# Kernel tuning notes

Hardware: AMD Instinct MI355X
Metric: run time of the kernel (lower is better)

Reference implementation:

```python
import jax, jax.numpy as jnp
import numpy as np

N, E, G = 100000, 1600000, 16
GW = 128
EPS = 1e-5        # BatchNorm eps
MIN_SCORE = 0.1   # TopK min_score
TOL = 1e-7        # PyG topk tolerance
NEG = -1e9


def _seg_sum(v, idx, n):
    return jax.ops.segment_sum(v, idx, num_segments=n)


def _seg_max(v, idx, n):
    return jax.ops.segment_max(v, idx, num_segments=n)


def setup_inputs():
    ks = jax.random.split(jax.random.key(0), 32)
    inp = {}
    inp['x'] = jax.random.normal(ks[0], (N, 2), jnp.float32)
    inp['edge_index'] = jax.random.randint(ks[1], (2, E), 0, N, jnp.int32)
    inp['batch_index'] = jnp.sort(jax.random.randint(ks[2], (N,), 0, G, jnp.int32))
    inp['gcn_w'] = jax.random.normal(ks[3], (2, 1), jnp.float32) / np.sqrt(2.0)
    inp['gcn_b'] = jax.random.normal(ks[4], (1,), jnp.float32) * 0.1
    inp['topk_w'] = jax.random.normal(ks[5], (1,), jnp.float32)
    dims = [(2, GW), (GW, GW), (GW, GW)]
    j = 6
    for i, (din, dout) in enumerate(dims):
        s = 1.0 / np.sqrt(din)
        inp[f'cheb{i}_w0'] = jax.random.normal(ks[j], (din, dout), jnp.float32) * s; j += 1
        inp[f'cheb{i}_w1'] = jax.random.normal(ks[j], (din, dout), jnp.float32) * s; j += 1
        inp[f'cheb{i}_b'] = jax.random.normal(ks[j], (dout,), jnp.float32) * 0.1; j += 1
    inp['bn_gamma'] = jax.random.uniform(ks[j], (3, GW), jnp.float32) + 0.5; j += 1
    inp['bn_beta'] = jax.random.normal(ks[j], (3, GW), jnp.float32) * 0.1; j += 1
    inp['bn_mean'] = jax.random.normal(ks[j], (3, GW), jnp.float32) * 0.1; j += 1
    inp['bn_var'] = jax.random.uniform(ks[j], (3, GW), jnp.float32) + 0.5; j += 1
    for name, (din, dout) in [('lin0', (3 * GW, 32)), ('lin1', (32, 8)), ('linf', (8, 3))]:
        s = 1.0 / np.sqrt(din)
        inp[f'{name}_w'] = jax.random.normal(ks[j], (din, dout), jnp.float32) * s; j += 1
        inp[f'{name}_b'] = jax.random.normal(ks[j], (dout,), jnp.float32) * s; j += 1
    return inp


def reference(x, edge_index, batch_index, gcn_w, gcn_b, topk_w,
              cheb0_w0, cheb0_w1, cheb0_b, cheb1_w0, cheb1_w1, cheb1_b,
              cheb2_w0, cheb2_w1, cheb2_b, bn_gamma, bn_beta, bn_mean, bn_var,
              lin0_w, lin0_b, lin1_w, lin1_b, linf_w, linf_b):
    src, dst = edge_index[0], edge_index[1]

    # --- CustomGCN(2,1): sym-normalized A+I (frozen weights), out [N,1] ---
    xw = x @ gcn_w                                  # [N,1]
    deg = _seg_sum(jnp.ones(E, x.dtype), dst, N) + 1.0   # +1 self loop
    dinv = jax.lax.rsqrt(deg)
    agg = _seg_sum(xw[src] * (dinv[src] * dinv[dst])[:, None], dst, N)
    attn = agg + xw * (dinv * dinv)[:, None] + gcn_b

    # --- CustomTopK(1, min_score=0.1): per-graph softmax, keep > min(max-tol, 0.1) ---
    s_raw = (attn * topk_w).sum(-1)                 # [N]
    smax = _seg_max(s_raw, batch_index, G)
    ex = jnp.exp(s_raw - smax[batch_index])
    score = ex / _seg_sum(ex, batch_index, G)[batch_index]
    thr = jnp.minimum(_seg_max(score, batch_index, G) - TOL, MIN_SCORE)[batch_index]
    mask = score > thr                              # [N] kept nodes
    fm = mask.astype(x.dtype)
    h = x * score[:, None] * fm[:, None]            # x[perm] * score[perm], masked form

    # edges surviving the pooling (both endpoints kept)
    em = fm[src] * fm[dst]                          # [E]
    degf = _seg_sum(em, dst, N)
    dinvf = jnp.where(degf > 0, jax.lax.rsqrt(jnp.maximum(degf, 1.0)), 0.0)
    normf = dinvf[src] * dinvf[dst] * em            # [E] sym-norm on filtered graph

    def cheb(h, w0, w1, b):
        # K=2, lambda_max=2: Tx1 = (L_hat) h = -D^-1/2 A D^-1/2 h
        tx1 = -_seg_sum(h[src] * normf[:, None], dst, N)
        return h @ w0 + tx1 @ w1 + b

    def bn(h, i):
        return (h - bn_mean[i]) * (bn_gamma[i] * jax.lax.rsqrt(bn_var[i] + EPS)) + bn_beta[i]

    mneg = jnp.where(mask[:, None], 0.0, NEG)       # mask dropped nodes out of gmp
    xs = []
    for i, (w0, w1, b) in enumerate([(cheb0_w0, cheb0_w1, cheb0_b),
                                     (cheb1_w0, cheb1_w1, cheb1_b),
                                     (cheb2_w0, cheb2_w1, cheb2_b)]):
        h = jax.nn.elu(cheb(h, w0, w1, b))
        h = bn(h, i)
        xs.append(jnp.maximum(_seg_max(h + mneg, batch_index, G), NEG))
    g = jnp.concatenate(xs, axis=1)                 # [G, 3*GW]

    g = jax.nn.elu(g @ lin0_w + lin0_b)
    g = jax.nn.elu(g @ lin1_w + lin1_b)
    # dropout is identity in eval mode
    g = g @ linf_w + linf_b
    return jax.nn.log_softmax(g, axis=1)
```

## Files before the change

kernel.cpp:

```cpp
#include <hip/hip_runtime.h>
#include <math.h>

#define NG 16
#define GW 128
#define NEGV -1.0e9f
#define EPSBN 1e-5f
#define MIN_SCORE 0.1f
#define TOLK 1e-7f
#define NBIN 1024
#define NPBMAX 256
#define EPT 4
#define KCAP 256
#define ECAP 2048
#define ROWCAP 16
#define LECAP 256

__device__ __forceinline__ unsigned encf(float f) {
  unsigned u = __float_as_uint(f);
  return (u & 0x80000000u) ? ~u : (u | 0x80000000u);
}
__device__ __forceinline__ float decf(unsigned u) {
  unsigned b = (u & 0x80000000u) ? (u & 0x7fffffffu) : ~u;
  return __uint_as_float(b);
}
__device__ __forceinline__ float eluf(float v) { return v > 0.0f ? v : expm1f(v); }

__device__ __forceinline__ void stage_w(const float* __restrict__ w, float* wbuf, int t) {
  const float4* w4 = (const float4*)w;
  float4* b4 = (float4*)wbuf;
  #pragma unroll
  for (int i = 0; i < 16; ++i) b4[t + 256 * i] = w4[t + 256 * i];
}

__global__ void k_zero(int* __restrict__ bincnt, int* __restrict__ counters,
                       unsigned* __restrict__ smax_e, float* __restrict__ sumex) {
  int t = threadIdx.x;
  for (int i = t; i < NBIN; i += blockDim.x) bincnt[i] = 0;
  if (t < NG) { smax_e[t] = encf(-INFINITY); sumex[t] = 0.0f; }
  if (t == 0) { counters[0] = 0; counters[1] = 0; }
}

__global__ __launch_bounds__(1024) void k_scatter(
    const int* __restrict__ src, const int* __restrict__ dst, int ne, int shift,
    int cap, int* __restrict__ bincnt, unsigned* __restrict__ sorted,
    const float* __restrict__ x, const float* __restrict__ gcn_w,
    float* __restrict__ xw, int n) {
  __shared__ int lh[NBIN];
  __shared__ int gb[NBIN];
  int t = threadIdx.x;
  long gid = (long)blockIdx.x * 1024 + t;
  long gs = (long)gridDim.x * 1024;
  float w0 = gcn_w[0], w1 = gcn_w[1];
  for (long i = gid; i < n; i += gs) xw[i] = x[2 * i] * w0 + x[2 * i + 1] * w1;
  for (int b = t; b < NBIN; b += 1024) lh[b] = 0;
// ... 153 lines not shown
  const uint4* s4 = (const uint4*)(sorted + (size_t)b * cap);
  int cnt = bincnt[b]; if (cnt > cap) cnt = cap;
  int nv = cnt >> 2;
  auto proc = [&](unsigned p) {
    int ks = kmap[p & 0xFFFFFFu];
    if (ks < 0) return;
    int kd = kmap[off + (int)(p >> 24)];
    if (kd < 0) return;
    int j = atomicAdd(&counters[1], 1);
    if (j < ECAP) {
      eks[j] = ks;
      ekd[j] = kd;
      atomicAdd(&degfc[kd], 1.0f);
    }
  };
  for (int i = threadIdx.x; i < nv; i += blockDim.x) {
    uint4 p = s4[i];
    proc(p.x); proc(p.y); proc(p.z); proc(p.w);
  }
  const unsigned* ss = sorted + (size_t)b * cap;
  for (int i = (nv << 2) + threadIdx.x; i < cnt; i += blockDim.x) proc(ss[i]);
}

__device__ void tail_layer_slow(const float* hin, float* tx, float* hout,
                                const float* __restrict__ w0, const float* __restrict__ w1,
                                const float* __restrict__ cb,
                                const float* __restrict__ bng, const float* __restrict__ bnb,
                                const float* __restrict__ bnm, const float* __restrict__ bnv,
                                int L, int R, int S,
                                const int* kl, const int* rows_g,
                                const int* __restrict__ kbatch,
                                const int* __restrict__ eks, const int* __restrict__ ekd,
                                const float* __restrict__ degfc,
                                unsigned* lgm, int g, int t) {
  for (int i = t; i < R * GW; i += 256) tx[i] = 0.0f;
  __syncthreads();
  for (int e = t; e < S; e += 256) {
    int kd = ekd[e];
    int dr = kl[kd];
    if (dr < 0) continue;
    int sr = kl[eks[e]];
    if (sr < 0) continue;
    float dfs = degfc[eks[e]], dfd = degfc[kd];
    float nf = (dfs > 0.f ? rsqrtf(dfs) : 0.f) * (dfd > 0.f ? rsqrtf(dfd) : 0.f);
    for (int c = 0; c < GW; ++c)
      atomicAdd(&tx[dr * GW + c], -hin[sr * GW + c] * nf);
  }
  __syncthreads();
  int j = t & 127, ih = t >> 7;
  float sc = bng[L * GW + j] * rsqrtf(bnv[L * GW + j] + EPSBN);
  float mn = bnm[L * GW + j], bt = bnb[L * GW + j], bj = cb[j];
  for (int i = ih; i < R; i += 2) {
    float acc = bj;
    for (int k = 0; k < GW; ++k)
      acc += hin[i * GW + k] * w0[k * GW + j] + tx[i * GW + k] * w1[k * GW + j];
    float v = eluf(acc);
    v = (v - mn) * sc + bt;
    if (hout) hout[i * GW + j] = v;
    if (kbatch[rows_g[i]] == g) atomicMax(&lgm[L * GW + j], encf(v));
  }
  __syncthreads();
}

template <int MR>
__device__ void layer_fast(const float* hin, const float* txl, float* hout,
                           const float* __restrict__ w0g, const float* __restrict__ w1g,
                           const float* __restrict__ cb,
                           const float* __restrict__ bng, const float* __restrict__ bnb,
                           const float* __restrict__ bnm, const float* __restrict__ bnv,
                           int L, int R, const int* rows_g,
                           const int* __restrict__ kbatch,
                           unsigned* lgm, float* wbuf, int g, int t) {
  int j = t & 127, ih = t >> 7;
  float bj = cb[j];
  float acc[MR];
  #pragma unroll
  for (int r = 0; r < MR; ++r) acc[r] = bj;
  stage_w(w0g, wbuf, t);
  __syncthreads();
  for (int k = 0; k < GW; ++k) {
    float wv = wbuf[k * GW + j];
    #pragma unroll
    for (int r = 0; r < MR; ++r) {
      int row = ih + 2 * r;
      if (row < R) acc[r] += hin[row * GW + k] * wv;
    }
  }
  __syncthreads();
  stage_w(w1g, wbuf, t);
  __syncthreads();
  for (int k = 0; k < GW; ++k) {
    float wv = wbuf[k * GW + j];
    #pragma unroll
    for (int r = 0; r < MR; ++r) {
      int row = ih + 2 * r;
      if (row < R) acc[r] += txl[row * GW + k] * wv;
    }
  }
  float sc = bng[L * GW + j] * rsqrtf(bnv[L * GW + j] + EPSBN);
  float mn = bnm[L * GW + j], bt = bnb[L * GW + j];
  #pragma unroll
  for (int r = 0; r < MR; ++r) {
    int row = ih + 2 * r;
    if (row < R) {
      float v = eluf(acc[r]);
      v = (v - mn) * sc + bt;
      if (hout) hout[row * GW + j] = v;
      if (kbatch[rows_g[row]] == g) atomicMax(&lgm[L * GW + j], encf(v));
    }
  }
  __syncthreads();
}

__global__ __launch_bounds__(256) void k_tail(
    const float* __restrict__ hk, const int* __restrict__ kbatch,
    const int* __restrict__ counters,
    const int* __restrict__ eks, const int* __restrict__ ekd,
    const float* __restrict__ degfc,
    const float* __restrict__ c0w0, const float* __restrict__ c0w1, const float* __restrict__ c0b,
    const float* __restrict__ c1w0, const float* __restrict__ c1w1, const float* __restrict__ c1b,
    const float* __restrict__ c2w0, const float* __restrict__ c2w1, const float* __restrict__ c2b,
    const float* __restrict__ bng, const float* __restrict__ bnb,
    const float* __restrict__ bnm, const float* __restrict__ bnv,
    const float* __restrict__ l0w, const float* __restrict__ l0b,
    const float* __restrict__ l1w, const float* __restrict__ l1b,
    const float* __restrict__ lfw, const float* __restrict__ lfb,
    float* __restrict__ g_hA, float* __restrict__ g_hB, float* __restrict__ g_tx,
    float* __restrict__ g_t0, float* __restrict__ out) {
  __shared__ float wbuf[GW * GW];
  __shared__ float sA[ROWCAP * GW], sB[ROWCAP * GW], sT[ROWCAP * GW];
  __shared__ float t0v[ROWCAP * 2];
  __shared__ int kl[KCAP];
  __shared__ int rows_g[KCAP];
  __shared__ int les[LECAP], led[LECAP];
  __shared__ float lenf[LECAP];
  __shared__ unsigned lgm[3 * GW];
  __shared__ int cnts[2];
  __shared__ float red[256];
  __shared__ float mlp0[32], mlp1[8], lg3[3];

  int g = blockIdx.x, t = threadIdx.x;
  int K = counters[0]; if (K > KCAP) K = KCAP;
  int S = counters[1]; if (S > ECAP) S = ECAP;
  if (t == 0) { cnts[0] = 0; cnts[1] = 0; }
  for (int i = t; i < KCAP; i += 256) kl[i] = -1;
  for (int i = t; i < 3 * GW; i += 256) lgm[i] = encf(NEGV);
  __syncthreads();
  for (int i = t; i < K; i += 256)
    if (kbatch[i] == g) { int r = atomicAdd(&cnts[0], 1); rows_g[r] = i; }
  __syncthreads();
  int R0 = cnts[0];
  for (int r = t; r < R0; r += 256) kl[rows_g[r]] = r;
  __syncthreads();
  if (t == 0) {
    for (int pass = 0; pass < 2; ++pass) {
      int Rcur = cnts[0];
      for (int e = 0; e < S; ++e) {
        int kd = ekd[e];
        if (kl[kd] >= 0 && kl[kd] < Rcur) {
          int ks = eks[e];
          if (kl[ks] < 0) { int r = cnts[0]++; rows_g[r] = ks; kl[ks] = r; }
        }
      }
    }
  }
  __syncthreads();
  int R = cnts[0];
  for (int e = t; e < S; e += 256) {
    int kd = ekd[e];
    if (kl[kd] >= 0) {
      int j = atomicAdd(&cnts[1], 1);
      if (j < LECAP) {
        les[j] = eks[e];
        led[j] = kl[kd];
        float dfs = degfc[eks[e]], dfd = degfc[kd];
        lenf[j] = (dfs > 0.f ? rsqrtf(dfs) : 0.f) * (dfd > 0.f ? rsqrtf(dfd) : 0.f);
      }
    }
  }
  __syncthreads();
  int LE = cnts[1]; if (LE > LECAP) LE = LECAP;
  bool fast = (R <= ROWCAP) && (cnts[1] <= LECAP);

  if (fast) {
    for (int i = t; i < R * 2; i += 256) t0v[i] = 0.0f;
    __syncthreads();
    for (int idx = t; idx < LE * 2; idx += 256) {
      int e = idx >> 1, c = idx & 1;
      atomicAdd(&t0v[led[e] * 2 + c], -hk[les[e] * 2 + c] * lenf[e]);
    }
    __syncthreads();
    {
      int j = t & 127, ih = t >> 7;
      float sc = bng[j] * rsqrtf(bnv[j] + EPSBN);
      float mn = bnm[j], bt = bnb[j];
      for (int i = ih; i < R; i += 2) {
        int gi = rows_g[i];
        float acc = c0b[j] + hk[gi * 2] * c0w0[j] + hk[gi * 2 + 1] * c0w0[GW + j]
                  + t0v[i * 2] * c0w1[j] + t0v[i * 2 + 1] * c0w1[GW + j];
        float v = eluf(acc);
        v = (v - mn) * sc + bt;
        sA[i * GW + j] = v;
        if (kbatch[gi] == g) atomicMax(&lgm[j], encf(v));
      }
    }
    __syncthreads();
    for (int i = t; i < R * GW; i += 256) sT[i] = 0.0f;
    __syncthreads();
    for (int idx = t; idx < LE * GW; idx += 256) {
      int e = idx >> 7, c = idx & 127;
      int sr = kl[les[e]];
      if (sr >= 0) atomicAdd(&sT[led[e] * GW + c], -sA[sr * GW + c] * lenf[e]);
    }
    __syncthreads();
    if (R <= 2)
      layer_fast<1>(sA, sT, sB, c1w0, c1w1, c1b, bng, bnb, bnm, bnv, 1, R,
                    rows_g, kbatch, lgm, wbuf, g, t);
    else
      layer_fast<8>(sA, sT, sB, c1w0, c1w1, c1b, bng, bnb, bnm, bnv, 1, R,
                    rows_g, kbatch, lgm, wbuf, g, t);
    for (int i = t; i < R * GW; i += 256) sT[i] = 0.0f;
    __syncthreads();
    for (int idx = t; idx < LE * GW; idx += 256) {
      int e = idx >> 7, c = idx & 127;
      int sr = kl[les[e]];
      if (sr >= 0) atomicAdd(&sT[led[e] * GW + c], -sB[sr * GW + c] * lenf[e]);
    }
    __syncthreads();
    if (R <= 2)
      layer_fast<1>(sB, sT, nullptr, c2w0, c2w1, c2b, bng, bnb, bnm, bnv, 2, R,
                    rows_g, kbatch, lgm, wbuf, g, t);
    else
      layer_fast<8>(sB, sT, nullptr, c2w0, c2w1, c2b, bng, bnb, bnm, bnv, 2, R,
                    rows_g, kbatch, lgm, wbuf, g, t);
  } else {
    float* hA  = g_hA + (size_t)g * KCAP * GW;
    float* hB  = g_hB + (size_t)g * KCAP * GW;
    float* tx  = g_tx + (size_t)g * KCAP * GW;
    float* t0p = g_t0 + (size_t)g * KCAP * 2;
    for (int i = t; i < R * 2; i += 256) t0p[i] = 0.0f;
    __syncthreads();
    for (int e = t; e < S; e += 256) {
      int kd = ekd[e];
      int dr = kl[kd];
      if (dr < 0) continue;
      int ks = eks[e];
      float dfs = degfc[ks], dfd = degfc[kd];
      float nf = (dfs > 0.f ? rsqrtf(dfs) : 0.f) * (dfd > 0.f ? rsqrtf(dfd) : 0.f);
      atomicAdd(&t0p[dr * 2],     -hk[ks * 2] * nf);
      atomicAdd(&t0p[dr * 2 + 1], -hk[ks * 2 + 1] * nf);
    }
    __syncthreads();
    {
      int j = t & 127, ih = t >> 7;
      float sc = bng[j] * rsqrtf(bnv[j] + EPSBN);
      float mn = bnm[j], bt = bnb[j];
      for (int i = ih; i < R; i += 2) {
        int gi = rows_g[i];
        float acc = c0b[j] + hk[gi * 2] * c0w0[j] + hk[gi * 2 + 1] * c0w0[GW + j]
                  + t0p[i * 2] * c0w1[j] + t0p[i * 2 + 1] * c0w1[GW + j];
        float v = eluf(acc);
        v = (v - mn) * sc + bt;
        hA[i * GW + j] = v;
        if (kbatch[gi] == g) atomicMax(&lgm[j], encf(v));
      }
    }
    __syncthreads();
    tail_layer_slow(hA, tx, hB, c1w0, c1w1, c1b, bng, bnb, bnm, bnv, 1, R, S,
                    kl, rows_g, kbatch, eks, ekd, degfc, lgm, g, t);
    tail_layer_slow(hB, tx, nullptr, c2w0, c2w1, c2b, bng, bnb, bnm, bnv, 2, R, S,
                    kl, rows_g, kbatch, eks, ekd, degfc, lgm, g, t);
  }

  {
    const float4* a4 = (const float4*)l0w;
    float4* b4 = (float4*)wbuf;
    #pragma unroll
    for (int i = 0; i < 12; ++i) b4[t + 256 * i] = a4[t + 256 * i];
    wbuf[12288 + t] = l1w[t & 255];
    if (t < 24) wbuf[12544 + t] = lfw[t];
  }
  __syncthreads();
  {
    int jo = t & 31, kb = t >> 5;
    float a = 0.f;
    for (int kk = 0; kk < 48; ++kk) {
      int k = kb * 48 + kk;
      a += decf(lgm[k]) * wbuf[k * 32 + jo];
    }
    red[t] = a;
  }
  __syncthreads();
  if (t < 32) {
    float acc = l0b[t];
    for (int b2 = 0; b2 < 8; ++b2) acc += red[b2 * 32 + t];
    mlp0[t] = eluf(acc);
  }
  __syncthreads();
  if (t < 8) {
    float acc = l1b[t];
    for (int k = 0; k < 32; ++k) acc += mlp0[k] * wbuf[12288 + k * 8 + t];
    mlp1[t] = eluf(acc);
  }
  __syncthreads();
  if (t < 3) {
    float acc = lfb[t];
    for (int k = 0; k < 8; ++k) acc += mlp1[k] * wbuf[12544 + k * 3 + t];
    lg3[t] = acc;
  }
  __syncthreads();
  if (t == 0) {
    float a = lg3[0], b = lg3[1], c = lg3[2];
    float m = fmaxf(a, fmaxf(b, c));
    float ls = m + logf(expf(a - m) + expf(b - m) + expf(c - m));
    out[g * 3 + 0] = a - ls;
    out[g * 3 + 1] = b - ls;
    out[g * 3 + 2] = c - ls;
  }
}

extern "C" void kernel_launch(void* const* d_in, const int* in_sizes, int n_in,
                              void* d_out, int out_size, void* d_ws, size_t ws_size,
                              hipStream_t stream) {
  const float* x      = (const float*)d_in[0];
  const int*   ei     = (const int*)d_in[1];
  const int*   batch  = (const int*)d_in[2];
  const float* gcn_w  = (const float*)d_in[3];
  const float* gcn_b  = (const float*)d_in[4];
  const float* topk_w = (const float*)d_in[5];
  const float* c0w0 = (const float*)d_in[6],  *c0w1 = (const float*)d_in[7],  *c0b = (const float*)d_in[8];
  const float* c1w0 = (const float*)d_in[9],  *c1w1 = (const float*)d_in[10], *c1b = (const float*)d_in[11];
  const float* c2w0 = (const float*)d_in[12], *c2w1 = (const float*)d_in[13], *c2b = (const float*)d_in[14];
  const float* bng = (const float*)d_in[15], *bnb = (const float*)d_in[16];
  const float* bnm = (const float*)d_in[17], *bnv = (const float*)d_in[18];
  const float* l0w = (const float*)d_in[19], *l0b = (const float*)d_in[20];
  const float* l1w = (const float*)d_in[21], *l1b = (const float*)d_in[22];
  const float* lfw = (const float*)d_in[23], *lfb = (const float*)d_in[24];
  float* out = (float*)d_out;

  const int n  = in_sizes[2];
  const int ne = in_sizes[1] / 2;
// ... 15 lines not shown
    off += (bytes + 255) & ~(size_t)255;
    return r;
  };
  float*    xw     = (float*)A((size_t)n * 4);
  float*    dinv   = (float*)A((size_t)n * 4);
  float*    y      = (float*)A((size_t)n * 4);
  float*    s_raw  = (float*)A((size_t)n * 4);
  int*      kmap   = (int*)A((size_t)n * 4);
  unsigned* sorted = (unsigned*)A((size_t)NBIN * cap * 4);
  int*      bincnt = (int*)A(NBIN * 4);
  unsigned* smax_e = (unsigned*)A(NG * 4);
  float*    sumex  = (float*)A(NG * 4);
  int*      counters = (int*)A(8);
  int*      kbatch = (int*)A((size_t)KCAP * 4);
  float*    degfc  = (float*)A((size_t)KCAP * 4);
  float*    hk     = (float*)A((size_t)KCAP * 8);
  int*      eks    = (int*)A((size_t)ECAP * 4);
  int*      ekd    = (int*)A((size_t)ECAP * 4);
  float*    g_hA   = (float*)A((size_t)NG * KCAP * GW * 4);
  float*    g_hB   = (float*)A((size_t)NG * KCAP * GW * 4);
  float*    g_tx   = (float*)A((size_t)NG * KCAP * GW * 4);
  float*    g_t0   = (float*)A((size_t)NG * KCAP * 8);

  const int nbN = (n + 255) / 256;
  const int nbS = (ne + 1024 * EPT - 1) / (1024 * EPT);

  k_zero<<<1, 1024, 0, stream>>>(bincnt, counters, smax_e, sumex);
  k_scatter<<<nbS, 1024, 0, stream>>>(src, dst, ne, shift, cap, bincnt, sorted,
                                      x, gcn_w, xw, n);
  k_c1<<<NBIN, 256, 0, stream>>>(sorted, bincnt, cap, xw, dinv, y, n, shift);
  k_c2<<<NBIN, 256, 0, stream>>>(sorted, bincnt, cap, y, xw, dinv, batch, gcn_b,
                                 topk_w, s_raw, smax_e, sumex, n, shift);
  k_compact_n<<<nbN, 256, 0, stream>>>(s_raw, sumex, smax_e, batch, x, kmap,
                                       kbatch, hk, degfc, counters, n);
  k_compact_e<<<NBIN, 256, 0, stream>>>(sorted, bincnt, cap, kmap, eks, ekd,
                                        degfc, counters, n, shift);
  k_tail<<<NG, 256, 0, stream>>>(hk, kbatch, counters, eks, ekd, degfc,
                                 c0w0, c0w1, c0b, c1w0, c1w1, c1b, c2w0, c2w1, c2b,
                                 bng, bnb, bnm, bnv, l0w, l0b, l1w, l1b, lfw, lfb,
                                 g_hA, g_hB, g_tx, g_t0, out);
}
```

Before: 100.9 us.

## Fuse all pipeline stages into one cooperative persistent kernel with grid syncs

Replaces the chain of seven kernel launches with a single cooperative kernel of 256 blocks that runs each stage (init, edge bucketing, degree, GCN scores, compaction, tail MLP) separated by grid.sync(). It also restructures shared memory into one 64KB buffer and stages weights in halves so everything fits. This removes per-launch overhead and the idle gaps between small kernels. In exchange it uses fewer blocks per stage, adds grid-wide barriers and holds a lot of shared memory, which limits occupancy. A fallback to the old launches is kept if the cooperative launch is unavailable.

```diff
diff --git a/kernel.cpp b/kernel.cpp
--- a/kernel.cpp
+++ b/kernel.cpp
@@ -1,5 +1,8 @@
 #include <hip/hip_runtime.h>
+#include <hip/hip_cooperative_groups.h>
 #include <math.h>
+
+namespace cg = cooperative_groups;
 
 #define NG 16
 #define GW 128
@@ -9,11 +12,14 @@
 #define TOLK 1e-7f
 #define NBIN 1024
 #define NPBMAX 256
-#define EPT 4
 #define KCAP 256
 #define ECAP 2048
 #define ROWCAP 16
 #define LECAP 256
+#define NBLK 256
+#define BT 256
+#define EPTS 32
+#define EPT 4
 
 __device__ __forceinline__ unsigned encf(float f) {
   unsigned u = __float_as_uint(f);
@@ -25,11 +31,530 @@
 }
 __device__ __forceinline__ float eluf(float v) { return v > 0.0f ? v : expm1f(v); }
 
-__device__ __forceinline__ void stage_w(const float* __restrict__ w, float* wbuf, int t) {
+__device__ __forceinline__ void stage_half(const float* __restrict__ w, float* wbuf, int t) {
   const float4* w4 = (const float4*)w;
   float4* b4 = (float4*)wbuf;
+  float4 r0 = w4[t],        r1 = w4[t + 256],  r2 = w4[t + 512],  r3 = w4[t + 768];
+  float4 r4 = w4[t + 1024], r5 = w4[t + 1280], r6 = w4[t + 1536], r7 = w4[t + 1792];
+  b4[t] = r0; b4[t + 256] = r1; b4[t + 512] = r2; b4[t + 768] = r3;
+  b4[t + 1024] = r4; b4[t + 1280] = r5; b4[t + 1536] = r6; b4[t + 1792] = r7;
+}
+
+template <int MR>
+__device__ void layer_fast(const float* hin, const float* txl, float* hout,
+                           const float* __restrict__ w0g, const float* __restrict__ w1g,
+                           const float* __restrict__ cb,
+                           const float* __restrict__ bng, const float* __restrict__ bnb,
+                           const float* __restrict__ bnm, const float* __restrict__ bnv,
+                           int L, int R, const int* rows_g,
+                           const int* __restrict__ kbatch,
+                           unsigned* lgm, float* wbuf, int g, int t) {
+  int j = t & 127, ih = t >> 7;
+  float bj = cb[j];
+  float acc[MR];
   #pragma unroll
-  for (int i = 0; i < 16; ++i) b4[t + 256 * i] = w4[t + 256 * i];
+  for (int r = 0; r < MR; ++r) acc[r] = bj;
+  for (int half = 0; half < 2; ++half) {
+    stage_half(w0g + half * 64 * GW, wbuf, t);
+    __syncthreads();
+    for (int k = 0; k < 64; ++k) {
+      float wv = wbuf[k * GW + j];
+      #pragma unroll
+      for (int r = 0; r < MR; ++r) {
+        int row = ih + 2 * r;
+        if (row < R) acc[r] += hin[row * GW + half * 64 + k] * wv;
+      }
+    }
+    __syncthreads();
+  }
+  for (int half = 0; half < 2; ++half) {
+    stage_half(w1g + half * 64 * GW, wbuf, t);
+    __syncthreads();
+    for (int k = 0; k < 64; ++k) {
+      float wv = wbuf[k * GW + j];
+      #pragma unroll
+      for (int r = 0; r < MR; ++r) {
+        int row = ih + 2 * r;
+        if (row < R) acc[r] += txl[row * GW + half * 64 + k] * wv;
+      }
+    }
+    __syncthreads();
+  }
+  float sc = bng[L * GW + j] * rsqrtf(bnv[L * GW + j] + EPSBN);
+  float mn = bnm[L * GW + j], bt = bnb[L * GW + j];
+  #pragma unroll
+  for (int r = 0; r < MR; ++r) {
+    int row = ih + 2 * r;
+    if (row < R) {
+      float v = eluf(acc[r]);
+      v = (v - mn) * sc + bt;
+      if (hout) hout[row * GW + j] = v;
+      if (kbatch[rows_g[row]] == g) atomicMax(&lgm[L * GW + j], encf(v));
+    }
+  }
+  __syncthreads();
+}
+
+__device__ void tail_layer_slow(const float* hin, float* tx, float* hout,
+                                const float* __restrict__ w0, const float* __restrict__ w1,
+                                const float* __restrict__ cb,
+                                const float* __restrict__ bng, const float* __restrict__ bnb,
+                                const float* __restrict__ bnm, const float* __restrict__ bnv,
+                                int L, int R, int S, int nthr,
+                                const int* kl, const int* rows_g,
+                                const int* __restrict__ kbatch,
+                                const int* __restrict__ eks, const int* __restrict__ ekd,
+                                const float* __restrict__ degfc,
+                                unsigned* lgm, int g, int t) {
+  for (int i = t; i < R * GW; i += nthr) tx[i] = 0.0f;
+  __syncthreads();
+  for (int e = t; e < S; e += nthr) {
+    int kd = ekd[e];
+    int dr = kl[kd];
+    if (dr < 0) continue;
+    int sr = kl[eks[e]];
+    if (sr < 0) continue;
+    float dfs = degfc[eks[e]], dfd = degfc[kd];
+    float nf = (dfs > 0.f ? rsqrtf(dfs) : 0.f) * (dfd > 0.f ? rsqrtf(dfd) : 0.f);
+    for (int c = 0; c < GW; ++c)
+      atomicAdd(&tx[dr * GW + c], -hin[sr * GW + c] * nf);
+  }
+  __syncthreads();
+  int j = t & 127, ih = t >> 7, rs = nthr >> 7;
+  float sc = bng[L * GW + j] * rsqrtf(bnv[L * GW + j] + EPSBN);
+  float mn = bnm[L * GW + j], bt = bnb[L * GW + j], bj = cb[j];
+  for (int i = ih; i < R; i += rs) {
+    float acc = bj;
+    for (int k = 0; k < GW; ++k)
+      acc += hin[i * GW + k] * w0[k * GW + j] + tx[i * GW + k] * w1[k * GW + j];
+    float v = eluf(acc);
+    v = (v - mn) * sc + bt;
+    if (hout) hout[i * GW + j] = v;
+    if (kbatch[rows_g[i]] == g) atomicMax(&lgm[L * GW + j], encf(v));
+  }
+  __syncthreads();
+}
+
+__device__ void tail_body(unsigned char* smem, int g, int t,
+                          const float* __restrict__ hk, const int* __restrict__ kbatch,
+                          const int* __restrict__ counters,
+                          const int* __restrict__ eks, const int* __restrict__ ekd,
+                          const float* __restrict__ degfc,
+                          const float* __restrict__ c0w0, const float* __restrict__ c0w1, const float* __restrict__ c0b,
+                          const float* __restrict__ c1w0, const float* __restrict__ c1w1, const float* __restrict__ c1b,
+                          const float* __restrict__ c2w0, const float* __restrict__ c2w1, const float* __restrict__ c2b,
+                          const float* __restrict__ bng, const float* __restrict__ bnb,
+                          const float* __restrict__ bnm, const float* __restrict__ bnv,
+                          const float* __restrict__ l0w, const float* __restrict__ l0b,
+                          const float* __restrict__ l1w, const float* __restrict__ l1b,
+                          const float* __restrict__ lfw, const float* __restrict__ lfb,
+                          float* __restrict__ g_hA, float* __restrict__ g_hB,
+                          float* __restrict__ g_tx, float* __restrict__ g_t0,
+                          float* __restrict__ out) {
+  float* wbuf   = (float*)smem;
+  float* sA     = (float*)(smem + 32768);
+  float* sB     = (float*)(smem + 40960);
+  float* sT     = (float*)(smem + 49152);
+  int*   kl     = (int*)(smem + 57344);
+  int*   rows_g = (int*)(smem + 58368);
+  int*   les    = (int*)(smem + 59392);
+  int*   led    = (int*)(smem + 60416);
+  float* lenf   = (float*)(smem + 61440);
+  unsigned* lgm = (unsigned*)(smem + 62464);
+  int*   cnts   = (int*)(smem + 64000);
+  float* t0v    = sT;
+  float* red    = sA;
+  float* mlp0   = sB;
+  float* mlp1   = (float*)(smem + 40960 + 128);
+  float* lg3    = (float*)(smem + 40960 + 160);
+
+  int K = counters[0]; if (K > KCAP) K = KCAP;
+  int S = counters[1]; if (S > ECAP) S = ECAP;
+  if (t == 0) { cnts[0] = 0; cnts[1] = 0; }
+  for (int i = t; i < KCAP; i += BT) kl[i] = -1;
+  for (int i = t; i < 3 * GW; i += BT) lgm[i] = encf(NEGV);
+  __syncthreads();
+  for (int i = t; i < K; i += BT)
+    if (kbatch[i] == g) { int r = atomicAdd(&cnts[0], 1); rows_g[r] = i; }
+  __syncthreads();
+  int R0 = cnts[0];
+  for (int r = t; r < R0; r += BT) kl[rows_g[r]] = r;
+  __syncthreads();
+  if (t == 0) {
+    for (int pass = 0; pass < 2; ++pass) {
+      int Rcur = cnts[0];
+      for (int e = 0; e < S; ++e) {
+        int kd = ekd[e];
+        if (kl[kd] >= 0 && kl[kd] < Rcur) {
+          int ks = eks[e];
+          if (kl[ks] < 0) { int r = cnts[0]++; rows_g[r] = ks; kl[ks] = r; }
+        }
+      }
+    }
+  }
+  __syncthreads();
+  int R = cnts[0];
+  for (int e = t; e < S; e += BT) {
+    int kd = ekd[e];
+    if (kl[kd] >= 0) {
+      int j = atomicAdd(&cnts[1], 1);
+      if (j < LECAP) {
+        les[j] = eks[e];
+        led[j] = kl[kd];
+        float dfs = degfc[eks[e]], dfd = degfc[kd];
+        lenf[j] = (dfs > 0.f ? rsqrtf(dfs) : 0.f) * (dfd > 0.f ? rsqrtf(dfd) : 0.f);
+      }
+    }
+  }
+  __syncthreads();
+  int LE = cnts[1]; if (LE > LECAP) LE = LECAP;
+  bool fast = (R <= ROWCAP) && (cnts[1] <= LECAP);
+
+  if (fast) {
+    for (int i = t; i < R * 2; i += BT) t0v[i] = 0.0f;
+    __syncthreads();
+    for (int idx = t; idx < LE * 2; idx += BT) {
+      int e = idx >> 1, c = idx & 1;
+      atomicAdd(&t0v[led[e] * 2 + c], -hk[les[e] * 2 + c] * lenf[e]);
+    }
+    __syncthreads();
+    {
+      int j = t & 127, ih = t >> 7;
+      float sc = bng[j] * rsqrtf(bnv[j] + EPSBN);
+      float mn = bnm[j], bt = bnb[j];
+      for (int i = ih; i < R; i += 2) {
+        int gi = rows_g[i];
+        float acc = c0b[j] + hk[gi * 2] * c0w0[j] + hk[gi * 2 + 1] * c0w0[GW + j]
+                  + t0v[i * 2] * c0w1[j] + t0v[i * 2 + 1] * c0w1[GW + j];
+        float v = eluf(acc);
+        v = (v - mn) * sc + bt;
+        sA[i * GW + j] = v;
+        if (kbatch[gi] == g) atomicMax(&lgm[j], encf(v));
+      }
+    }
+    __syncthreads();
+    for (int i = t; i < R * GW; i += BT) sT[i] = 0.0f;
+    __syncthreads();
+    for (int idx = t; idx < LE * GW; idx += BT) {
+      int e = idx >> 7, c = idx & 127;
+      int sr = kl[les[e]];
+      if (sr >= 0) atomicAdd(&sT[led[e] * GW + c], -sA[sr * GW + c] * lenf[e]);
+    }
+    __syncthreads();
+    if (R <= 2)
+      layer_fast<1>(sA, sT, sB, c1w0, c1w1, c1b, bng, bnb, bnm, bnv, 1, R,
+                    rows_g, kbatch, lgm, wbuf, g, t);
+    else
+      layer_fast<8>(sA, sT, sB, c1w0, c1w1, c1b, bng, bnb, bnm, bnv, 1, R,
+                    rows_g, kbatch, lgm, wbuf, g, t);
+    for (int i = t; i < R * GW; i += BT) sT[i] = 0.0f;
+    __syncthreads();
+    for (int idx = t; idx < LE * GW; idx += BT) {
+      int e = idx >> 7, c = idx & 127;
+      int sr = kl[les[e]];
+      if (sr >= 0) atomicAdd(&sT[led[e] * GW + c], -sB[sr * GW + c] * lenf[e]);
+    }
+    __syncthreads();
+    if (R <= 2)
+      layer_fast<1>(sB, sT, nullptr, c2w0, c2w1, c2b, bng, bnb, bnm, bnv, 2, R,
+                    rows_g, kbatch, lgm, wbuf, g, t);
+    else
+      layer_fast<8>(sB, sT, nullptr, c2w0, c2w1, c2b, bng, bnb, bnm, bnv, 2, R,
+                    rows_g, kbatch, lgm, wbuf, g, t);
+  } else {
+    float* hA  = g_hA + (size_t)g * KCAP * GW;
+    float* hB  = g_hB + (size_t)g * KCAP * GW;
+    float* tx  = g_tx + (size_t)g * KCAP * GW;
+    float* t0p = g_t0 + (size_t)g * KCAP * 2;
+    for (int i = t; i < R * 2; i += BT) t0p[i] = 0.0f;
+    __syncthreads();
+    for (int e = t; e < S; e += BT) {
+      int kd = ekd[e];
+      int dr = kl[kd];
+      if (dr < 0) continue;
+      int ks = eks[e];
+      float dfs = degfc[ks], dfd = degfc[kd];
+      float nf = (dfs > 0.f ? rsqrtf(dfs) : 0.f) * (dfd > 0.f ? rsqrtf(dfd) : 0.f);
+      atomicAdd(&t0p[dr * 2],     -hk[ks * 2] * nf);
+      atomicAdd(&t0p[dr * 2 + 1], -hk[ks * 2 + 1] * nf);
+    }
+    __syncthreads();
+    {
+      int j = t & 127, ih = t >> 7;
+      float sc = bng[j] * rsqrtf(bnv[j] + EPSBN);
+      float mn = bnm[j], bt = bnb[j];
+      for (int i = ih; i < R; i += 2) {
+        int gi = rows_g[i];
+        float acc = c0b[j] + hk[gi * 2] * c0w0[j] + hk[gi * 2 + 1] * c0w0[GW + j]
+                  + t0p[i * 2] * c0w1[j] + t0p[i * 2 + 1] * c0w1[GW + j];
+        float v = eluf(acc);
+        v = (v - mn) * sc + bt;
+        hA[i * GW + j] = v;
+        if (kbatch[gi] == g) atomicMax(&lgm[j], encf(v));
+      }
+    }
+    __syncthreads();
+    tail_layer_slow(hA, tx, hB, c1w0, c1w1, c1b, bng, bnb, bnm, bnv, 1, R, S, BT,
+                    kl, rows_g, kbatch, eks, ekd, degfc, lgm, g, t);
+    tail_layer_slow(hB, tx, nullptr, c2w0, c2w1, c2b, bng, bnb, bnm, bnv, 2, R, S, BT,
+                    kl, rows_g, kbatch, eks, ekd, degfc, lgm, g, t);
+  }
+
+  {
+    float a = 0.f;
+    int jo = t & 31, kb = t >> 5;
+    for (int half = 0; half < 2; ++half) {
+      const float4* a4 = (const float4*)(l0w + half * 6144);
+      float4* b4 = (float4*)wbuf;
+      float4 q0 = a4[t], q1 = a4[t + 256], q2 = a4[t + 512];
+      float4 q3 = a4[t + 768], q4 = a4[t + 1024], q5 = a4[t + 1280];
+      b4[t] = q0; b4[t + 256] = q1; b4[t + 512] = q2;
+      b4[t + 768] = q3; b4[t + 1024] = q4; b4[t + 1280] = q5;
+      __syncthreads();
+      #pragma unroll
+      for (int kk = 0; kk < 24; ++kk) {
+        int k = kb * 24 + kk;
+        a += decf(lgm[half * 192 + k]) * wbuf[k * 32 + jo];
+      }
+      __syncthreads();
+    }
+    red[t] = a;
+  }
+  __syncthreads();
+  if (t < 32) {
+    float acc = l0b[t];
+    for (int b2 = 0; b2 < 8; ++b2) acc += red[b2 * 32 + t];
+    mlp0[t] = eluf(acc);
+  }
+  __syncthreads();
+  if (t < 8) {
+    float acc = l1b[t];
+    for (int k = 0; k < 32; ++k) acc += mlp0[k] * l1w[k * 8 + t];
+    mlp1[t] = eluf(acc);
+  }
+  __syncthreads();
+  if (t < 3) {
+    float acc = lfb[t];
+    for (int k = 0; k < 8; ++k) acc += mlp1[k] * lfw[k * 3 + t];
+    lg3[t] = acc;
+  }
+  __syncthreads();
+  if (t == 0) {
+    float a = lg3[0], b = lg3[1], c = lg3[2];
+    float m = fmaxf(a, fmaxf(b, c));
+    float ls = m + logf(expf(a - m) + expf(b - m) + expf(c - m));
+    out[g * 3 + 0] = a - ls;
+    out[g * 3 + 1] = b - ls;
+    out[g * 3 + 2] = c - ls;
+  }
+}
+
+struct FP {
+  const int *src, *dst; int ne, n, shift, cap, ch;
+  const float *x; const int *batch;
+  const float *gcn_w, *gcn_b, *topk_w;
+  float *xw, *dinv, *y, *s_raw; int *kmap;
+  unsigned *sorted; int *bincnt; unsigned *smax_e; float *sumex; int *counters;
+  int *kbatch; float *degfc, *hk; int *eks, *ekd;
+  const float *c0w0, *c0w1, *c0b, *c1w0, *c1w1, *c1b, *c2w0, *c2w1, *c2b;
+  const float *bng, *bnb, *bnm, *bnv;
+  const float *l0w, *l0b, *l1w, *l1b, *lfw, *lfb;
+  float *g_hA, *g_hB, *g_tx, *g_t0;
+  float *out;
+};
+
+__global__ __launch_bounds__(BT) void k_fused(FP p) {
+  __shared__ __align__(16) unsigned char smem[65536];
+  cg::grid_group grid = cg::this_grid();
+  int t = threadIdx.x, bid = blockIdx.x;
+  int gid = bid * BT + t;
+  const int gs = NBLK * BT;
+
+  for (int i = gid; i < NBIN; i += gs) p.bincnt[i] = 0;
+  if (gid < NG) { p.smax_e[gid] = encf(-INFINITY); p.sumex[gid] = 0.f; }
+  if (gid == 0) { p.counters[0] = 0; p.counters[1] = 0; }
+  for (int i = gid; i < KCAP; i += gs) p.degfc[i] = 0.f;
+  {
+    float w0 = p.gcn_w[0], w1 = p.gcn_w[1];
+    for (int i = gid; i < p.n; i += gs) p.xw[i] = p.x[2 * i] * w0 + p.x[2 * i + 1] * w1;
+  }
+  grid.sync();
+
+  {
+    int* lh = (int*)smem;
+    int* gb = (int*)(smem + 4096);
+    for (int b = t; b < NBIN; b += BT) lh[b] = 0;
+    __syncthreads();
+    int base = bid * p.ch;
+    int lim = p.ne - base; if (lim > p.ch) lim = p.ch; if (lim < 0) lim = 0;
+    int rank[EPTS], dv[EPTS];
+    #pragma unroll
+    for (int k = 0; k < EPTS; ++k) {
+      int el = k * BT + t;
+      rank[k] = 0; dv[k] = 0;
+      if (el < lim) { dv[k] = p.dst[base + el]; rank[k] = atomicAdd(&lh[dv[k] >> p.shift], 1); }
+    }
+    __syncthreads();
+    for (int b = t; b < NBIN; b += BT)
+      gb[b] = lh[b] ? atomicAdd(&p.bincnt[b], lh[b]) : 0;
+    __syncthreads();
+    #pragma unroll
+    for (int k = 0; k < EPTS; ++k) {
+      int el = k * BT + t;
+      if (el < lim) {
+        int d = dv[k], bin = d >> p.shift;
+        int pos = gb[bin] + rank[k];
+        if (pos < p.cap)
+          p.sorted[(size_t)bin * p.cap + pos] =
+              ((unsigned)(d & ((1 << p.shift) - 1)) << 24) | (unsigned)p.src[base + el];
+      }
+    }
+  }
+  grid.sync();
+
+  {
+    int* ldeg = (int*)smem;
+    int npb = 1 << p.shift;
+    for (int b = bid; b < NBIN; b += NBLK) {
+      int off = b << p.shift;
+      for (int j2 = t; j2 < npb; j2 += BT) ldeg[j2] = 0;
+      __syncthreads();
+      if (off < p.n) {
+        const uint4* s4 = (const uint4*)(p.sorted + (size_t)b * p.cap);
+        int cnt = p.bincnt[b]; if (cnt > p.cap) cnt = p.cap;
+        int nv = cnt >> 2;
+        for (int i = t; i < nv; i += BT) {
+          uint4 q = s4[i];
+          atomicAdd(&ldeg[q.x >> 24], 1); atomicAdd(&ldeg[q.y >> 24], 1);
+          atomicAdd(&ldeg[q.z >> 24], 1); atomicAdd(&ldeg[q.w >> 24], 1);
+        }
+        const unsigned* ss = p.sorted + (size_t)b * p.cap;
+        for (int i = (nv << 2) + t; i < cnt; i += BT)
+          atomicAdd(&ldeg[ss[i] >> 24], 1);
+      }
+      __syncthreads();
+      if (off < p.n) {
+        for (int j2 = t; j2 < npb; j2 += BT) {
+          int g = off + j2;
+          if (g < p.n) {
+            float dvv = rsqrtf((float)(ldeg[j2] + 1));
+            p.dinv[g] = dvv;
+            p.y[g] = p.xw[g] * dvv;
+          }
+        }
+      }
+      __syncthreads();
+    }
+  }
+  grid.sync();
+
+  {
+    float* lt = (float*)smem;
+    unsigned* ls = (unsigned*)(smem + 1024);
+    float* lsum = (float*)(smem + 1088);
+    int npb = 1 << p.shift;
+    if (t < NG) { ls[t] = encf(-INFINITY); lsum[t] = 0.f; }
+    __syncthreads();
+    for (int b = bid; b < NBIN; b += NBLK) {
+      int off = b << p.shift;
+      for (int j2 = t; j2 < npb; j2 += BT) lt[j2] = 0.f;
+      __syncthreads();
+      if (off < p.n) {
+        const uint4* s4 = (const uint4*)(p.sorted + (size_t)b * p.cap);
+        int cnt = p.bincnt[b]; if (cnt > p.cap) cnt = p.cap;
+        int nv = cnt >> 2;
+        for (int i = t; i < nv; i += BT) {
+          uint4 q = s4[i];
+          float ya = p.y[q.x & 0xFFFFFFu], yb = p.y[q.y & 0xFFFFFFu];
+          float yc = p.y[q.z & 0xFFFFFFu], yd = p.y[q.w & 0xFFFFFFu];
+          atomicAdd(&lt[q.x >> 24], ya); atomicAdd(&lt[q.y >> 24], yb);
+          atomicAdd(&lt[q.z >> 24], yc); atomicAdd(&lt[q.w >> 24], yd);
+        }
+        const unsigned* ss = p.sorted + (size_t)b * p.cap;
+        for (int i = (nv << 2) + t; i < cnt; i += BT) {
+          unsigned q = ss[i];
+          atomicAdd(&lt[q >> 24], p.y[q & 0xFFFFFFu]);
+        }
+      }
+      __syncthreads();
+      if (off < p.n) {
+        float gb_ = p.gcn_b[0], tw = p.topk_w[0];
+        for (int j2 = t; j2 < npb; j2 += BT) {
+          int g = off + j2;
+          if (g < p.n) {
+            float dvv = p.dinv[g];
+            float attn = dvv * lt[j2] + p.xw[g] * dvv * dvv + gb_;
+            float s = attn * tw;
+            p.s_raw[g] = s;
+            int bb = p.batch[g];
+            atomicMax(&ls[bb], encf(s));
+            atomicAdd(&lsum[bb], expf(s));
+          }
+        }
+      }
+      __syncthreads();
+    }
+    if (t < NG) {
+      if (ls[t] != encf(-INFINITY)) atomicMax(&p.smax_e[t], ls[t]);
+      if (lsum[t] != 0.0f) atomicAdd(&p.sumex[t], lsum[t]);
+    }
+  }
+  grid.sync();
+
+  for (int i = gid; i < p.n; i += gs) {
+    int b = p.batch[i];
+    float se = p.sumex[b];
+    float score = expf(p.s_raw[i]) / se;
+    float ms = expf(decf(p.smax_e[b])) / se;
+    float thr = fminf(ms - TOLK, MIN_SCORE);
+    int m = -1;
+    if (score > thr) {
+      int idx = atomicAdd(&p.counters[0], 1);
+      if (idx < KCAP) {
+        m = idx;
+        p.kbatch[idx] = b;
+        p.hk[2 * idx]     = p.x[2 * i] * score;
+        p.hk[2 * idx + 1] = p.x[2 * i + 1] * score;
+      }
+    }
+    p.kmap[i] = m;
+  }
+  grid.sync();
+
+  {
+    for (int b = bid; b < NBIN; b += NBLK) {
+      int off = b << p.shift;
+      if (off >= p.n) continue;
+      const uint4* s4 = (const uint4*)(p.sorted + (size_t)b * p.cap);
+      int cnt = p.bincnt[b]; if (cnt > p.cap) cnt = p.cap;
+      int nv = cnt >> 2;
+      auto proc = [&](unsigned q) {
+        int ks = p.kmap[q & 0xFFFFFFu];
+        if (ks < 0) return;
+        int kd = p.kmap[off + (int)(q >> 24)];
+        if (kd < 0) return;
+        int j = atomicAdd(&p.counters[1], 1);
+        if (j < ECAP) {
+          p.eks[j] = ks;
+          p.ekd[j] = kd;
+          atomicAdd(&p.degfc[kd], 1.0f);
+        }
+      };
+      for (int i = t; i < nv; i += BT) {
+        uint4 q = s4[i];
+        proc(q.x); proc(q.y); proc(q.z); proc(q.w);
+      }
+      const unsigned* ss = p.sorted + (size_t)b * p.cap;
+      for (int i = (nv << 2) + t; i < cnt; i += BT) proc(ss[i]);
+    }
+  }
+  grid.sync();
+
+  if (bid < NG)
+    tail_body(smem, bid, t, p.hk, p.kbatch, p.counters, p.eks, p.ekd, p.degfc,
+              p.c0w0, p.c0w1, p.c0b, p.c1w0, p.c1w1, p.c1b, p.c2w0, p.c2w1, p.c2b,
+              p.bng, p.bnb, p.bnm, p.bnv, p.l0w, p.l0b, p.l1w, p.l1b, p.lfw, p.lfb,
+              p.g_hA, p.g_hB, p.g_tx, p.g_t0, p.out);
 }
 
 __global__ void k_zero(int* __restrict__ bincnt, int* __restrict__ counters,
@@ -229,97 +754,7 @@
   for (int i = (nv << 2) + threadIdx.x; i < cnt; i += blockDim.x) proc(ss[i]);
 }
 
-__device__ void tail_layer_slow(const float* hin, float* tx, float* hout,
-                                const float* __restrict__ w0, const float* __restrict__ w1,
-                                const float* __restrict__ cb,
-                                const float* __restrict__ bng, const float* __restrict__ bnb,
-                                const float* __restrict__ bnm, const float* __restrict__ bnv,
-                                int L, int R, int S,
-                                const int* kl, const int* rows_g,
-                                const int* __restrict__ kbatch,
-                                const int* __restrict__ eks, const int* __restrict__ ekd,
-                                const float* __restrict__ degfc,
-                                unsigned* lgm, int g, int t) {
-  for (int i = t; i < R * GW; i += 256) tx[i] = 0.0f;
-  __syncthreads();
-  for (int e = t; e < S; e += 256) {
-    int kd = ekd[e];
-    int dr = kl[kd];
-    if (dr < 0) continue;
-    int sr = kl[eks[e]];
-    if (sr < 0) continue;
-    float dfs = degfc[eks[e]], dfd = degfc[kd];
-    float nf = (dfs > 0.f ? rsqrtf(dfs) : 0.f) * (dfd > 0.f ? rsqrtf(dfd) : 0.f);
-    for (int c = 0; c < GW; ++c)
-      atomicAdd(&tx[dr * GW + c], -hin[sr * GW + c] * nf);
-  }
-  __syncthreads();
-  int j = t & 127, ih = t >> 7;
-  float sc = bng[L * GW + j] * rsqrtf(bnv[L * GW + j] + EPSBN);
-  float mn = bnm[L * GW + j], bt = bnb[L * GW + j], bj = cb[j];
-  for (int i = ih; i < R; i += 2) {
-    float acc = bj;
-    for (int k = 0; k < GW; ++k)
-      acc += hin[i * GW + k] * w0[k * GW + j] + tx[i * GW + k] * w1[k * GW + j];
-    float v = eluf(acc);
-    v = (v - mn) * sc + bt;
-    if (hout) hout[i * GW + j] = v;
-    if (kbatch[rows_g[i]] == g) atomicMax(&lgm[L * GW + j], encf(v));
-  }
-  __syncthreads();
-}
-
-template <int MR>
-__device__ void layer_fast(const float* hin, const float* txl, float* hout,
-                           const float* __restrict__ w0g, const float* __restrict__ w1g,
-                           const float* __restrict__ cb,
-                           const float* __restrict__ bng, const float* __restrict__ bnb,
-                           const float* __restrict__ bnm, const float* __restrict__ bnv,
-                           int L, int R, const int* rows_g,
-                           const int* __restrict__ kbatch,
-                           unsigned* lgm, float* wbuf, int g, int t) {
-  int j = t & 127, ih = t >> 7;
-  float bj = cb[j];
-  float acc[MR];
-  #pragma unroll
-  for (int r = 0; r < MR; ++r) acc[r] = bj;
-  stage_w(w0g, wbuf, t);
-  __syncthreads();
-  for (int k = 0; k < GW; ++k) {
-    float wv = wbuf[k * GW + j];
-    #pragma unroll
-    for (int r = 0; r < MR; ++r) {
-      int row = ih + 2 * r;
-      if (row < R) acc[r] += hin[row * GW + k] * wv;
-    }
-  }
-  __syncthreads();
-  stage_w(w1g, wbuf, t);
-  __syncthreads();
-  for (int k = 0; k < GW; ++k) {
-    float wv = wbuf[k * GW + j];
-    #pragma unroll
-    for (int r = 0; r < MR; ++r) {
-      int row = ih + 2 * r;
-      if (row < R) acc[r] += txl[row * GW + k] * wv;
-    }
-  }
-  float sc = bng[L * GW + j] * rsqrtf(bnv[L * GW + j] + EPSBN);
-  float mn = bnm[L * GW + j], bt = bnb[L * GW + j];
-  #pragma unroll
-  for (int r = 0; r < MR; ++r) {
-    int row = ih + 2 * r;
-    if (row < R) {
-      float v = eluf(acc[r]);
-      v = (v - mn) * sc + bt;
-      if (hout) hout[row * GW + j] = v;
-      if (kbatch[rows_g[row]] == g) atomicMax(&lgm[L * GW + j], encf(v));
-    }
-  }
-  __syncthreads();
-}
-
-__global__ __launch_bounds__(256) void k_tail(
+__global__ __launch_bounds__(BT) void k_tail(
     const float* __restrict__ hk, const int* __restrict__ kbatch,
     const int* __restrict__ counters,
     const int* __restrict__ eks, const int* __restrict__ ekd,
@@ -334,196 +769,11 @@
     const float* __restrict__ lfw, const float* __restrict__ lfb,
     float* __restrict__ g_hA, float* __restrict__ g_hB, float* __restrict__ g_tx,
     float* __restrict__ g_t0, float* __restrict__ out) {
-  __shared__ float wbuf[GW * GW];
-  __shared__ float sA[ROWCAP * GW], sB[ROWCAP * GW], sT[ROWCAP * GW];
-  __shared__ float t0v[ROWCAP * 2];
-  __shared__ int kl[KCAP];
-  __shared__ int rows_g[KCAP];
-  __shared__ int les[LECAP], led[LECAP];
-  __shared__ float lenf[LECAP];
-  __shared__ unsigned lgm[3 * GW];
-  __shared__ int cnts[2];
-  __shared__ float red[256];
-  __shared__ float mlp0[32], mlp1[8], lg3[3];
-
-  int g = blockIdx.x, t = threadIdx.x;
-  int K = counters[0]; if (K > KCAP) K = KCAP;
-  int S = counters[1]; if (S > ECAP) S = ECAP;
-  if (t == 0) { cnts[0] = 0; cnts[1] = 0; }
-  for (int i = t; i < KCAP; i += 256) kl[i] = -1;
-  for (int i = t; i < 3 * GW; i += 256) lgm[i] = encf(NEGV);
-  __syncthreads();
-  for (int i = t; i < K; i += 256)
-    if (kbatch[i] == g) { int r = atomicAdd(&cnts[0], 1); rows_g[r] = i; }
-  __syncthreads();
-  int R0 = cnts[0];
-  for (int r = t; r < R0; r += 256) kl[rows_g[r]] = r;
-  __syncthreads();
-  if (t == 0) {
-    for (int pass = 0; pass < 2; ++pass) {
-      int Rcur = cnts[0];
-      for (int e = 0; e < S; ++e) {
-        int kd = ekd[e];
-        if (kl[kd] >= 0 && kl[kd] < Rcur) {
-          int ks = eks[e];
-          if (kl[ks] < 0) { int r = cnts[0]++; rows_g[r] = ks; kl[ks] = r; }
-        }
-      }
-    }
-  }
-  __syncthreads();
-  int R = cnts[0];
-  for (int e = t; e < S; e += 256) {
-    int kd = ekd[e];
-    if (kl[kd] >= 0) {
-      int j = atomicAdd(&cnts[1], 1);
-      if (j < LECAP) {
-        les[j] = eks[e];
-        led[j] = kl[kd];
-        float dfs = degfc[eks[e]], dfd = degfc[kd];
-        lenf[j] = (dfs > 0.f ? rsqrtf(dfs) : 0.f) * (dfd > 0.f ? rsqrtf(dfd) : 0.f);
-      }
-    }
-  }
-  __syncthreads();
-  int LE = cnts[1]; if (LE > LECAP) LE = LECAP;
-  bool fast = (R <= ROWCAP) && (cnts[1] <= LECAP);
-
-  if (fast) {
-    for (int i = t; i < R * 2; i += 256) t0v[i] = 0.0f;
-    __syncthreads();
-    for (int idx = t; idx < LE * 2; idx += 256) {
-      int e = idx >> 1, c = idx & 1;
-      atomicAdd(&t0v[led[e] * 2 + c], -hk[les[e] * 2 + c] * lenf[e]);
-    }
-    __syncthreads();
-    {
-      int j = t & 127, ih = t >> 7;
-      float sc = bng[j] * rsqrtf(bnv[j] + EPSBN);
-      float mn = bnm[j], bt = bnb[j];
-      for (int i = ih; i < R; i += 2) {
-        int gi = rows_g[i];
-        float acc = c0b[j] + hk[gi * 2] * c0w0[j] + hk[gi * 2 + 1] * c0w0[GW + j]
-                  + t0v[i * 2] * c0w1[j] + t0v[i * 2 + 1] * c0w1[GW + j];
-        float v = eluf(acc);
-        v = (v - mn) * sc + bt;
-        sA[i * GW + j] = v;
-        if (kbatch[gi] == g) atomicMax(&lgm[j], encf(v));
-      }
-    }
-    __syncthreads();
-    for (int i = t; i < R * GW; i += 256) sT[i] = 0.0f;
-    __syncthreads();
-    for (int idx = t; idx < LE * GW; idx += 256) {
-      int e = idx >> 7, c = idx & 127;
-      int sr = kl[les[e]];
-      if (sr >= 0) atomicAdd(&sT[led[e] * GW + c], -sA[sr * GW + c] * lenf[e]);
-    }
-    __syncthreads();
-    if (R <= 2)
-      layer_fast<1>(sA, sT, sB, c1w0, c1w1, c1b, bng, bnb, bnm, bnv, 1, R,
-                    rows_g, kbatch, lgm, wbuf, g, t);
-    else
-      layer_fast<8>(sA, sT, sB, c1w0, c1w1, c1b, bng, bnb, bnm, bnv, 1, R,
-                    rows_g, kbatch, lgm, wbuf, g, t);
-    for (int i = t; i < R * GW; i += 256) sT[i] = 0.0f;
-    __syncthreads();
-    for (int idx = t; idx < LE * GW; idx += 256) {
-      int e = idx >> 7, c = idx & 127;
-      int sr = kl[les[e]];
-      if (sr >= 0) atomicAdd(&sT[led[e] * GW + c], -sB[sr * GW + c] * lenf[e]);
-    }
-    __syncthreads();
-    if (R <= 2)
-      layer_fast<1>(sB, sT, nullptr, c2w0, c2w1, c2b, bng, bnb, bnm, bnv, 2, R,
-                    rows_g, kbatch, lgm, wbuf, g, t);
-    else
-      layer_fast<8>(sB, sT, nullptr, c2w0, c2w1, c2b, bng, bnb, bnm, bnv, 2, R,
-                    rows_g, kbatch, lgm, wbuf, g, t);
-  } else {
-    float* hA  = g_hA + (size_t)g * KCAP * GW;
-    float* hB  = g_hB + (size_t)g * KCAP * GW;
-    float* tx  = g_tx + (size_t)g * KCAP * GW;
-    float* t0p = g_t0 + (size_t)g * KCAP * 2;
-    for (int i = t; i < R * 2; i += 256) t0p[i] = 0.0f;
-    __syncthreads();
-    for (int e = t; e < S; e += 256) {
-      int kd = ekd[e];
-      int dr = kl[kd];
-      if (dr < 0) continue;
-      int ks = eks[e];
-      float dfs = degfc[ks], dfd = degfc[kd];
-      float nf = (dfs > 0.f ? rsqrtf(dfs) : 0.f) * (dfd > 0.f ? rsqrtf(dfd) : 0.f);
-      atomicAdd(&t0p[dr * 2],     -hk[ks * 2] * nf);
-      atomicAdd(&t0p[dr * 2 + 1], -hk[ks * 2 + 1] * nf);
-    }
-    __syncthreads();
-    {
-      int j = t & 127, ih = t >> 7;
-      float sc = bng[j] * rsqrtf(bnv[j] + EPSBN);
-      float mn = bnm[j], bt = bnb[j];
-      for (int i = ih; i < R; i += 2) {
-        int gi = rows_g[i];
-        float acc = c0b[j] + hk[gi * 2] * c0w0[j] + hk[gi * 2 + 1] * c0w0[GW + j]
-                  + t0p[i * 2] * c0w1[j] + t0p[i * 2 + 1] * c0w1[GW + j];
-        float v = eluf(acc);
-        v = (v - mn) * sc + bt;
-        hA[i * GW + j] = v;
-        if (kbatch[gi] == g) atomicMax(&lgm[j], encf(v));
-      }
-    }
-    __syncthreads();
-    tail_layer_slow(hA, tx, hB, c1w0, c1w1, c1b, bng, bnb, bnm, bnv, 1, R, S,
-                    kl, rows_g, kbatch, eks, ekd, degfc, lgm, g, t);
-    tail_layer_slow(hB, tx, nullptr, c2w0, c2w1, c2b, bng, bnb, bnm, bnv, 2, R, S,
-                    kl, rows_g, kbatch, eks, ekd, degfc, lgm, g, t);
-  }
-
-  {
-    const float4* a4 = (const float4*)l0w;
-    float4* b4 = (float4*)wbuf;
-    #pragma unroll
-    for (int i = 0; i < 12; ++i) b4[t + 256 * i] = a4[t + 256 * i];
-    wbuf[12288 + t] = l1w[t & 255];
-    if (t < 24) wbuf[12544 + t] = lfw[t];
-  }
-  __syncthreads();
-  {
-    int jo = t & 31, kb = t >> 5;
-    float a = 0.f;
-    for (int kk = 0; kk < 48; ++kk) {
-      int k = kb * 48 + kk;
-      a += decf(lgm[k]) * wbuf[k * 32 + jo];
-    }
-    red[t] = a;
-  }
-  __syncthreads();
-  if (t < 32) {
-    float acc = l0b[t];
-    for (int b2 = 0; b2 < 8; ++b2) acc += red[b2 * 32 + t];
-    mlp0[t] = eluf(acc);
-  }
-  __syncthreads();
-  if (t < 8) {
-    float acc = l1b[t];
-    for (int k = 0; k < 32; ++k) acc += mlp0[k] * wbuf[12288 + k * 8 + t];
-    mlp1[t] = eluf(acc);
-  }
-  __syncthreads();
-  if (t < 3) {
-    float acc = lfb[t];
-    for (int k = 0; k < 8; ++k) acc += mlp1[k] * wbuf[12544 + k * 3 + t];
-    lg3[t] = acc;
-  }
-  __syncthreads();
-  if (t == 0) {
-    float a = lg3[0], b = lg3[1], c = lg3[2];
-    float m = fmaxf(a, fmaxf(b, c));
-    float ls = m + logf(expf(a - m) + expf(b - m) + expf(c - m));
-    out[g * 3 + 0] = a - ls;
-    out[g * 3 + 1] = b - ls;
-    out[g * 3 + 2] = c - ls;
-  }
+  __shared__ __align__(16) unsigned char smem[65536];
+  tail_body(smem, blockIdx.x, threadIdx.x, hk, kbatch, counters, eks, ekd, degfc,
+            c0w0, c0w1, c0b, c1w0, c1w1, c1b, c2w0, c2w1, c2b,
+            bng, bnb, bnm, bnv, l0w, l0b, l1w, l1b, lfw, lfb,
+            g_hA, g_hB, g_tx, g_t0, out);
 }
 
 extern "C" void kernel_launch(void* const* d_in, const int* in_sizes, int n_in,
@@ -585,21 +835,50 @@
   float*    g_tx   = (float*)A((size_t)NG * KCAP * GW * 4);
   float*    g_t0   = (float*)A((size_t)NG * KCAP * 8);
 
-  const int nbN = (n + 255) / 256;
-  const int nbS = (ne + 1024 * EPT - 1) / (1024 * EPT);
-
-  k_zero<<<1, 1024, 0, stream>>>(bincnt, counters, smax_e, sumex);
-  k_scatter<<<nbS, 1024, 0, stream>>>(src, dst, ne, shift, cap, bincnt, sorted,
-                                      x, gcn_w, xw, n);
-  k_c1<<<NBIN, 256, 0, stream>>>(sorted, bincnt, cap, xw, dinv, y, n, shift);
-  k_c2<<<NBIN, 256, 0, stream>>>(sorted, bincnt, cap, y, xw, dinv, batch, gcn_b,
-                                 topk_w, s_raw, smax_e, sumex, n, shift);
-  k_compact_n<<<nbN, 256, 0, stream>>>(s_raw, sumex, smax_e, batch, x, kmap,
-                                       kbatch, hk, degfc, counters, n);
-  k_compact_e<<<NBIN, 256, 0, stream>>>(sorted, bincnt, cap, kmap, eks, ekd,
-                                        degfc, counters, n, shift);
-  k_tail<<<NG, 256, 0, stream>>>(hk, kbatch, counters, eks, ekd, degfc,
-                                 c0w0, c0w1, c0b, c1w0, c1w1, c1b, c2w0, c2w1, c2b,
-                                 bng, bnb, bnm, bnv, l0w, l0b, l1w, l1b, lfw, lfb,
-                                 g_hA, g_hB, g_tx, g_t0, out);
-}
+  int coop = 0;
+  {
+    int dev = 0;
+    hipGetDevice(&dev);
+    hipDeviceGetAttribute(&coop, hipDeviceAttributeCooperativeLaunch, dev);
+  }
+  const int ch = (ne + NBLK - 1) / NBLK;
+  bool done = false;
+  if (coop && ch <= EPTS * BT) {
+    FP p;
+    p.src = src; p.dst = dst; p.ne = ne; p.n = n; p.shift = shift; p.cap = cap; p.ch = ch;
+    p.x = x; p.batch = batch; p.gcn_w = gcn_w; p.gcn_b = gcn_b; p.topk_w = topk_w;
+    p.xw = xw; p.dinv = dinv; p.y = y; p.s_raw = s_raw; p.kmap = kmap;
+    p.sorted = sorted; p.bincnt = bincnt; p.smax_e = smax_e; p.sumex = sumex;
+    p.counters = counters; p.kbatch = kbatch; p.degfc = degfc; p.hk = hk;
+    p.eks = eks; p.ekd = ekd;
+    p.c0w0 = c0w0; p.c0w1 = c0w1; p.c0b = c0b;
+    p.c1w0 = c1w0; p.c1w1 = c1w1; p.c1b = c1b;
+    p.c2w0 = c2w0; p.c2w1 = c2w1; p.c2b = c2b;
+    p.bng = bng; p.bnb = bnb; p.bnm = bnm; p.bnv = bnv;
+    p.l0w = l0w; p.l0b = l0b; p.l1w = l1w; p.l1b = l1b; p.lfw = lfw; p.lfb = lfb;
+    p.g_hA = g_hA; p.g_hB = g_hB; p.g_tx = g_tx; p.g_t0 = g_t0;
+    p.out = out;
+    void* kargs[] = { &p };
+    hipError_t rc = hipLaunchCooperativeKernel((void*)k_fused, dim3(NBLK), dim3(BT),
+                                               kargs, 0, stream);
+    done = (rc == hipSuccess);
+  }
+  if (!done) {
+    const int nbN = (n + 255) / 256;
+    const int nbS = (ne + 1024 * EPT - 1) / (1024 * EPT);
+    k_zero<<<1, 1024, 0, stream>>>(bincnt, counters, smax_e, sumex);
+    k_scatter<<<nbS, 1024, 0, stream>>>(src, dst, ne, shift, cap, bincnt, sorted,
+                                        x, gcn_w, xw, n);
+    k_c1<<<NBIN, 256, 0, stream>>>(sorted, bincnt, cap, xw, dinv, y, n, shift);
+    k_c2<<<NBIN, 256, 0, stream>>>(sorted, bincnt, cap, y, xw, dinv, batch, gcn_b,
+                                   topk_w, s_raw, smax_e, sumex, n, shift);
+    k_compact_n<<<nbN, 256, 0, stream>>>(s_raw, sumex, smax_e, batch, x, kmap,
+                                         kbatch, hk, degfc, counters, n);
+    k_compact_e<<<NBIN, 256, 0, stream>>>(sorted, bincnt, cap, kmap, eks, ekd,
+                                          degfc, counters, n, shift);
+    k_tail<<<NG, BT, 0, stream>>>(hk, kbatch, counters, eks, ekd, degfc,
+                                  c0w0, c0w1, c0b, c1w0, c1w1, c1b, c2w0, c2w1, c2b,
+                                  bng, bnb, bnm, bnv, l0w, l0b, l1w, l1b, lfw, lfb,
+                                  g_hA, g_hB, g_tx, g_t0, out);
+  }
+}
```

Result: slower. 289.1 us (+186.6%).
